# Optimization experiments

Measured on AMD Instinct MI355X. Metric: run time of the kernel, lower is better.

The kernel has to match this reference:

```python
import jax, jax.numpy as jnp
import numpy as np

IMAGE_SIZE = 256
DET = int(IMAGE_SIZE * 2 ** 0.5 + 0.5)  # 362 detector bins (diagonal coverage)
US = 4
N_ACQ = 45                     # acquired views: 0,4,...,176 degrees
N_FULL = (N_ACQ - 1) * US + 1  # 177 full (upsampled) views


def setup_inputs() -> dict:
    key = jax.random.key(0)
    k1, k2 = jax.random.split(key)
    x_source = jax.random.normal(k1, (2, 1, IMAGE_SIZE, IMAGE_SIZE), jnp.float32)
    s_target = jax.random.normal(k2, (2, 1, DET, N_ACQ), jnp.float32)
    theta_acq = np.arange(0, 180, 4, dtype=np.float64)  # 45 acquired angles
    segs = [np.linspace(theta_acq[i], theta_acq[i + 1], US + 1)[:-1] for i in range(N_ACQ - 1)]
    theta_full = np.concatenate(segs + [theta_acq[-1:]]).astype(np.float32)  # [177]
    acq_idx = (np.arange(N_ACQ) * US).astype(np.int32)  # positions of acquired angles in theta_full
    return {"x_source": x_source, "s_target": s_target,
            "thetas_deg": jnp.asarray(theta_full), "acq_idx": jnp.asarray(acq_idx)}


def bilinear_gather(img, xs, ys):
    # img: [B,C,H,W]; xs, ys: pixel coords [A,det,det]; zero outside the image.
    H, W = img.shape[-2], img.shape[-1]
    x0 = jnp.floor(xs); y0 = jnp.floor(ys)
    wx = xs - x0; wy = ys - y0
    x0i = x0.astype(jnp.int32); y0i = y0.astype(jnp.int32)

    def get(yi, xi):
        valid = (xi >= 0) & (xi < W) & (yi >= 0) & (yi < H)
        v = img[:, :, jnp.clip(yi, 0, H - 1), jnp.clip(xi, 0, W - 1)]  # [B,C,A,det,det]
        return jnp.where(valid, v, 0.0)

    return (get(y0i, x0i) * (1 - wy) * (1 - wx)
            + get(y0i, x0i + 1) * (1 - wy) * wx
            + get(y0i + 1, x0i) * wy * (1 - wx)
            + get(y0i + 1, x0i + 1) * wy * wx)


def radon(x, thetas_rad, det):
    # Ray-sum projection: sino[theta, t] = sum_s image(t*cos - s*sin, t*sin + s*cos)
    B, C, H, W = x.shape
    t = jnp.arange(det, dtype=x.dtype) - (det - 1) / 2.0  # centered detector/ray coord
    cos = jnp.cos(thetas_rad)[:, None, None]
    sin = jnp.sin(thetas_rad)[:, None, None]
    T = t[None, :, None]; S = t[None, None, :]
    xs = T * cos - S * sin + (W - 1) / 2.0  # [A,det,det]
    ys = T * sin + S * cos + (H - 1) / 2.0
    return bilinear_gather(x, xs, ys).sum(-1)  # [B,C,A,det]


def ramp_filter(size):
    # skimage/pytorch_radon style ramp built from its real-space kernel
    n = np.concatenate([np.arange(1, size // 2 + 1, 2), np.arange(size // 2 - 1, 0, -2)])
    f = np.zeros(size)
    f[0] = 0.25
    f[1::2] = -1.0 / (np.pi * n) ** 2
    return jnp.asarray(2 * np.real(np.fft.fft(f)), dtype=jnp.float32)


def fbp(sino, thetas_rad, image_size):
    # Filtered back-projection. sino: [B,C,det,A]
    B, C, det, A = sino.shape
    pad = max(64, int(2 ** np.ceil(np.log2(2 * det))))
    filt = ramp_filter(pad)  # [pad]
    sp = jnp.pad(sino, ((0, 0), (0, 0), (0, pad - det), (0, 0)))
    sf = jnp.fft.ifft(jnp.fft.fft(sp, axis=2) * filt[None, None, :, None], axis=2).real
    sf = jnp.transpose(sf[:, :, :det, :], (0, 1, 3, 2)).astype(sino.dtype)  # [B,C,A,det]
    g = jnp.arange(image_size, dtype=sino.dtype) - (image_size - 1) / 2.0
    cos = jnp.cos(thetas_rad); sin = jnp.sin(thetas_rad)
    # detector coordinate hit by each pixel, per angle: t = x*cos + y*sin
    t = (cos[:, None, None] * g[None, None, :]
         + sin[:, None, None] * g[None, :, None] + (det - 1) / 2.0)  # [A,H,W]
    t = t.reshape(A, -1)
    t0 = jnp.floor(t)
    w = t - t0
    t0i = t0.astype(jnp.int32)
    aidx = jnp.arange(A)[:, None]

    def samp(ti):
        valid = (ti >= 0) & (ti < det)
        return jnp.where(valid, sf[:, :, aidx, jnp.clip(ti, 0, det - 1)], 0.0)  # [B,C,A,HW]

    v = samp(t0i) * (1 - w) + samp(t0i + 1) * w
    reco = v.sum(2) * (jnp.pi / (2 * A))
    return reco.reshape(B, C, image_size, image_size)


def reference(x_source, s_target, thetas_deg, acq_idx):
    th = thetas_deg * (jnp.pi / 180.0)
    s = radon(x_source, th, DET)          # [B,C,A,det]
    s = jnp.transpose(s, (0, 1, 3, 2))    # [B,C,det,A] -- angle axis last, as in the module
    # masked data-consistency update: acquired columns become (target - predicted)
    s = s.at[..., acq_idx].set(s_target - s[..., acq_idx])
    return fbp(s, th, IMAGE_SIZE)
```

## Files before the change

### kernel.cpp

```cpp
#include <hip/hip_runtime.h>
#include <math.h>

#define IMG   256
#define NFULL 177
#define DETN  362
#define NACQ  45
#define PAD   1024

#define SINO_OFF 0
#define SF_OFF   131072

#define HALF_T 180.5f
#define SEGL   32
#define TILE_W 1664

__constant__ const int kStripOrd[46] =
    {22,23,21,24,20,25,19,26,18,27,17,28,16,29,15,30,14,31,13,32,
     12,33,11,34,10,35,9,36,8,37,7,38,6,39,5,40,4,41,3,42,2,43,1,44,0,45};

__device__ __forceinline__ void gload16(const float* g, float* l) {
    __builtin_amdgcn_global_load_lds(
        (const __attribute__((address_space(1))) void*)g,
        (__attribute__((address_space(3))) void*)l, 16, 0, 0);
}

template<int P>
__device__ __forceinline__ float2 radon_strip2(
    const float* __restrict__ img0,
    const float* __restrict__ img1,
    float* tb,
    const float c, const float s,
    const float xbase, const float ybase,
    const float xAB_mn, const float yAB_mn, const float yAB_mx,
    const int Slo, const int Shi, const int lane)
{
    constexpr int W4   = P / 4;
    constexpr int HMAX = TILE_W / P;
    const int ts = lane & 7;
    float val0 = 0.0f, val1 = 0.0f;

    for (int Sseg = Slo; Sseg < Shi; Sseg += SEGL) {
        const float sv0 = (float)Sseg - HALF_T;
        const float sv1 = sv0 + (float)(SEGL - 1);
        const float xmn = xAB_mn - sv1 * s;
        const float ya  = sv0 * c, yb = sv1 * c;
        const float ymn = yAB_mn + fminf(ya, yb);
        const float ymx = yAB_mx + fmaxf(ya, yb);
        const int ix0  = (int)floorf(xmn) - 1;
        const int iy0  = (int)floorf(ymn) - 1;
        const int ix0a = ix0 & ~3;
        const int h    = min((int)floorf(ymx) + 3 - iy0, HMAX);
        const int total4 = W4 * h;
        const int nfull  = total4 & ~63;
        const bool interior = (ix0a >= 0) & (iy0 >= 0) &
                              (ix0a + P <= IMG) & (iy0 + h <= IMG);

        asm volatile("s_waitcnt lgkmcnt(0)" ::: "memory");

        if (interior) {
            const int base0 = iy0 * IMG + ix0a;
            for (int f0 = 0; f0 < nfull; f0 += 64) {
                const int f  = f0 + lane;
                const int r  = f / W4;
                const int c4 = f - r * W4;
                const int go = base0 + r * IMG + (c4 << 2);
                gload16(img0 + go, tb + (f0 << 2));
                gload16(img1 + go, tb + TILE_W + (f0 << 2));
            }
            const int f = nfull + lane;
            if (f < total4) {
                const int r  = f / W4;
                const int c4 = f - r * W4;
                const int go = base0 + r * IMG + (c4 << 2);
                gload16(img0 + go, tb + (nfull << 2));
                gload16(img1 + go, tb + TILE_W + (nfull << 2));
            }
        } else {
            for (int f = lane; f < total4; f += 64) {
                const int r  = f / W4;
                const int c4 = f - r * W4;
                const int gy = iy0 + r;
                const int gx = ix0a + (c4 << 2);
                const bool ok = ((unsigned)gy < (unsigned)IMG) &
                                ((unsigned)gx <= (unsigned)(IMG - 4));
                float4 v0 = make_float4(0.f, 0.f, 0.f, 0.f);
                float4 v1 = v0;
                if (ok) {
                    const int go = gy * IMG + gx;
                    v0 = *(const float4*)(img0 + go);
                    v1 = *(const float4*)(img1 + go);
                }
                *(float4*)(tb + (f << 2)) = v0;
                *(float4*)(tb + TILE_W + (f << 2)) = v1;
            }
        }
        asm volatile("s_waitcnt vmcnt(0) lgkmcnt(0)" ::: "memory");
        __builtin_amdgcn_sched_barrier(0);

        const float xoff = xbase - (float)ix0a;
        const float yoff = ybase - (float)iy0;
        const int Send = min(Sseg + SEGL, Shi);

        auto samp = [&](float sval) {
            const float xs  = fmaf(-sval, s, xoff);
            const float ys  = fmaf(sval, c, yoff);
            const float x0f = floorf(xs);
            const float y0f = floorf(ys);
            const float wx  = xs - x0f;
            const float wy  = ys - y0f;
            const int base = (int)fmaf(y0f, (float)P, x0f);
            const float a00 = tb[base];
            const float a01 = tb[base + 1];
            const float a10 = tb[base + P];
            const float a11 = tb[base + P + 1];
            const float b00 = tb[TILE_W + base];
            const float b01 = tb[TILE_W + base + 1];
            const float b10 = tb[TILE_W + base + P];
            const float b11 = tb[TILE_W + base + P + 1];
            const float ah0 = fmaf(wx, a01 - a00, a00);
            const float ah1 = fmaf(wx, a11 - a10, a10);
            val0 += fmaf(wy, ah1 - ah0, ah0);
            const float bh0 = fmaf(wx, b01 - b00, b00);
            const float bh1 = fmaf(wx, b11 - b10, b10);
            val1 += fmaf(wy, bh1 - bh0, bh0);
        };

        if (Send - Sseg == SEGL) {
            const float s0 = (float)(Sseg + ts) - HALF_T;
            #pragma unroll
            for (int u = 0; u < SEGL / 8; ++u) samp(s0 + (float)(8 * u));
        } else {
            for (int S = Sseg + ts; S < Send; S += 8) samp((float)S - HALF_T);
        }
    }
    return make_float2(val0, val1);
}

__global__ __launch_bounds__(64, 4) void radon_kernel(
    const float* __restrict__ x,
    const float* __restrict__ thetas,
    float* __restrict__ sino)
{
    const int a = blockIdx.x;
    const int lane = threadIdx.x & 63;
    const int sp   = kStripOrd[blockIdx.y];
    const int T0   = sp << 3;
    const int tt   = lane >> 3;
    const int ts   = lane & 7;
    const int T    = T0 + tt;

    __shared__ __align__(16) float tile[2 * TILE_W];

    const float th = thetas[a] * (float)(M_PI / 180.0);
    const float c = cosf(th);
    const float s = sinf(th);
    const float cx = (IMG - 1) * 0.5f;
    const float cy = (IMG - 1) * 0.5f;
    const float Tc = (float)T - HALF_T;
    const float xbase = Tc * c + cx;
    const float ybase = Tc * s + cy;

    float lo = -1e30f, hi = 1e30f;
    bool empty = (T >= DETN);
    {   const float aa = -s;
        if (aa > 1e-5f)       { lo = fmaxf(lo, (-1.0f - xbase) / aa); hi = fminf(hi, (256.0f - xbase) / aa); }
        else if (aa < -1e-5f) { lo = fmaxf(lo, (256.0f - xbase) / aa); hi = fminf(hi, (-1.0f - xbase) / aa); }
        else if (xbase <= -1.0f || xbase >= 256.0f) empty = true;
    }
    {   const float aa = c;
        if (aa > 1e-5f)       { lo = fmaxf(lo, (-1.0f - ybase) / aa); hi = fminf(hi, (256.0f - ybase) / aa); }
        else if (aa < -1e-5f) { lo = fmaxf(lo, (256.0f - ybase) / aa); hi = fminf(hi, (-1.0f - ybase) / aa); }
        else if (ybase <= -1.0f || ybase >= 256.0f) empty = true;
    }
    lo = fmaxf(lo, -200.0f);
    hi = fminf(hi, 200.0f);
    int Slo = max(0, (int)floorf(lo + HALF_T) - 1);
    int Shi = min(DETN, (int)floorf(hi + HALF_T) + 2);
    if (empty || Shi < Slo) { Slo = 0; Shi = 0; }

    int wlo = (Shi > Slo) ? Slo : DETN;
    int whi = (Shi > Slo) ? Shi : 0;
    #pragma unroll
    for (int d = 1; d < 64; d <<= 1) {
        wlo = min(wlo, __shfl_xor(wlo, d, 64));
        whi = max(whi, __shfl_xor(whi, d, 64));
    }

    int best = 2;
    {
        const float ac = fabsf(c), as = fabsf(s);
        const float spanx = 7.f * ac + 31.f * as;
        const float spany = 7.f * as + 31.f * ac;
        const float Pc[6] = {36.f, 40.f, 44.f, 48.f, 52.f, 56.f};
        const int   Hm[6] = {46, 41, 37, 34, 32, 29};
        int bcost = 1 << 30;
        #pragma unroll
        for (int p = 0; p < 6; ++p) {
            const float Pf = Pc[p];
            const float dT = s * Pf + c;
            const float dS = c * Pf - s;
            const int bank = (int)floorf((float)tt * dT + (float)ts * dS + 0.5f) & 31;
            unsigned long long m = ~0ull;
            #pragma unroll
            for (int bit = 0; bit < 5; ++bit) {
                const unsigned long long bb = __ballot((bank >> bit) & 1);
                m &= ((bank >> bit) & 1) ? bb : ~bb;
            }
            int cnt = __popcll(m);
            #pragma unroll
            for (int d = 1; d < 64; d <<= 1) cnt = max(cnt, __shfl_xor(cnt, d, 64));
            const bool fit = (spanx <= Pf - 8.05f) && (spany <= (float)Hm[p] - 5.05f);
            if (fit && cnt < bcost) { bcost = cnt; best = p; }
        }
    }

    const float TcA = (float)T0 - HALF_T;
    const float TcB = (float)(T0 + 7) - HALF_T;
    const float xAB_mn = fminf(TcA * c + cx, TcB * c + cx);
    const float yAB_mn = fminf(TcA * s + cy, TcB * s + cy);
    const float yAB_mx = fmaxf(TcA * s + cy, TcB * s + cy);

    const float* __restrict__ img0 = x;
    const float* __restrict__ img1 = x + IMG * IMG;

    float2 val;
    switch (best) {
    case 0:  val = radon_strip2<36>(img0, img1, tile, c, s, xbase, ybase,
                                    xAB_mn, yAB_mn, yAB_mx, wlo, whi, lane); break;
    case 1:  val = radon_strip2<40>(img0, img1, tile, c, s, xbase, ybase,
                                    xAB_mn, yAB_mn, yAB_mx, wlo, whi, lane); break;
    case 2:  val = radon_strip2<44>(img0, img1, tile, c, s, xbase, ybase,
                                    xAB_mn, yAB_mn, yAB_mx, wlo, whi, lane); break;
    case 3:  val = radon_strip2<48>(img0, img1, tile, c, s, xbase, ybase,
                                    xAB_mn, yAB_mn, yAB_mx, wlo, whi, lane); break;
    case 4:  val = radon_strip2<52>(img0, img1, tile, c, s, xbase, ybase,
                                    xAB_mn, yAB_mn, yAB_mx, wlo, whi, lane); break;
    default: val = radon_strip2<56>(img0, img1, tile, c, s, xbase, ybase,
                                    xAB_mn, yAB_mn, yAB_mx, wlo, whi, lane); break;
    }

    val.x += __shfl_xor(val.x, 1, 8);
    val.x += __shfl_xor(val.x, 2, 8);
    val.x += __shfl_xor(val.x, 4, 8);
    val.y += __shfl_xor(val.y, 1, 8);
    val.y += __shfl_xor(val.y, 2, 8);
    val.y += __shfl_xor(val.y, 4, 8);
    if (ts == 0 && T < DETN) {
        sino[a * DETN + T] = val.x;
        sino[(NFULL + a) * DETN + T] = val.y;
    }
}

__global__ __launch_bounds__(192) void dc_filter_kernel(
    const float* __restrict__ sino,
    const float* __restrict__ st,
    const int*   __restrict__ acq,
    float* __restrict__ sf)
{
    const int blk = blockIdx.x;
    const int b = blk / NFULL;
    const int a = blk - b * NFULL;
    const int tid = threadIdx.x;

    __shared__ float col[DETN];
    __shared__ float gf[PAD];

    const float SC = (float)(M_PI / (2.0 * NFULL));
    const float c0 = 0.5f * SC;
    for (int n = tid; n < PAD; n += 192) {
        float v = 0.0f;
        if (n & 1) {
            const int d = (n < PAD - n) ? n : (PAD - n);
            const float pd = (float)M_PI * (float)d;
            v = -2.0f / (pd * pd) * SC;
        }
        gf[n] = v;
    }

    int inv = -1;
    for (int i = 0; i < NACQ; ++i) {
        if (acq[i] == a) inv = i;
    }

    for (int m = tid; m < DETN; m += 192) {
        float val = sino[(b * NFULL + a) * DETN + m];
        if (inv >= 0) {
            val = st[(b * DETN + m) * NACQ + inv] - val;
        }
        col[m] = val;
    }
    __syncthreads();

    const int T = blockIdx.y * 181 + tid;
    if (tid < 181) {
        const int m0 = (T + 1) & 1;
        float acc = c0 * col[T];
        #pragma unroll 4
        for (int k = 0; k < 181; ++k) {
            const int m = m0 + 2 * k;
            acc += col[m] * gf[(T - m) & (PAD - 1)];
        }
        sf[(b * NFULL + a) * DETN + T] = acc;
    }
}

__global__ __launch_bounds__(256) void backproject_kernel(
    const float* __restrict__ sf,
    const float* __restrict__ thetas,
    float* __restrict__ out)
{
    __shared__ float cb[2 * NFULL];
    __shared__ float red[256];
    const int tid = threadIdx.x;
    const int lane  = tid & 63;
    const int phase = tid >> 6;
    const int pix = blockIdx.x * 64 + lane;
    const int b = pix >> 16;
    const int y = (pix >> 8) & 255;
    const int xq = pix & 255;
    const float gx = (float)xq - (IMG - 1) * 0.5f;
    const float gy = (float)y  - (IMG - 1) * 0.5f;

    for (int a = tid; a < NFULL; a += 256) {
        float th = thetas[a] * (float)(M_PI / 180.0);
        cb[2 * a]     = cosf(th);
        cb[2 * a + 1] = fmaf(sinf(th), gy, HALF_T);
    }
    __syncthreads();

    const float* __restrict__ sfb = sf + b * NFULL * DETN;

    float acc = 0.0f;
    #pragma unroll 4
    for (int a = phase; a < NFULL; a += 4) {
        const float cs = cb[2 * a];
        const float bs = cb[2 * a + 1];
        const float t = fmaf(cs, gx, bs);
        const float t0f = floorf(t);
        const float w = t - t0f;
        const float* row = sfb + a * DETN + (int)t0f;
        const float v0 = row[0];
        const float v1 = row[1];
        acc += v0 + w * (v1 - v0);
    }
    red[tid] = acc;
    __syncthreads();
    if (tid < 64) {
        out[blockIdx.x * 64 + tid] =
            red[tid] + red[tid + 64] + red[tid + 128] + red[tid + 192];
    }
}

extern "C" void kernel_launch(void* const* d_in, const int* in_sizes, int n_in,
                              void* d_out, int out_size, void* d_ws, size_t ws_size,
                              hipStream_t stream) {
    const float* x      = (const float*)d_in[0];
    const float* st     = (const float*)d_in[1];
    const float* thetas = (const float*)d_in[2];
    const int*   acq    = (const int*)d_in[3];
    float* out  = (float*)d_out;
    float* wsf  = (float*)d_ws;
    float* sino = wsf + SINO_OFF;
    float* sf   = wsf + SF_OFF;

    dim3 gA(NFULL, 46);
    radon_kernel<<<gA, 64, 0, stream>>>(x, thetas, sino);
    dim3 gB(2 * NFULL, 2);
    dc_filter_kernel<<<gB, 192, 0, stream>>>(sino, st, acq, sf);
    backproject_kernel<<<(2 * IMG * IMG) / 64, 256, 0, stream>>>(sf, thetas, out);
}
```

Baseline: 123.5 us.

## Prefetch next radon tile segment into registers while sampling current one

Replaces the direct global-to-LDS tile loads with a software pipeline in the radon strip loop. The next segment's image window is loaded into per-lane float4 registers (clamped addresses) before the current segment is sampled, and committed to LDS with out-of-bounds zeroing at the start of the next iteration. The goal is to hide global-memory latency behind the bilinear sampling work of a single-wave block. In exchange it uses many more VGPRs for staging, so launch bounds drop from 4 to 3 waves per SIMD, and it loses the cheaper interior fast path.

```diff
diff --git a/kernel.cpp b/kernel.cpp
--- a/kernel.cpp
+++ b/kernel.cpp
@@ -17,12 +17,6 @@
 __constant__ const int kStripOrd[46] =
     {22,23,21,24,20,25,19,26,18,27,17,28,16,29,15,30,14,31,13,32,
      12,33,11,34,10,35,9,36,8,37,7,38,6,39,5,40,4,41,3,42,2,43,1,44,0,45};
-
-__device__ __forceinline__ void gload16(const float* g, float* l) {
-    __builtin_amdgcn_global_load_lds(
-        (const __attribute__((address_space(1))) void*)g,
-        (__attribute__((address_space(3))) void*)l, 16, 0, 0);
-}
 
 template<int P>
 __device__ __forceinline__ float2 radon_strip2(
@@ -34,12 +28,16 @@
     const float xAB_mn, const float yAB_mn, const float yAB_mx,
     const int Slo, const int Shi, const int lane)
 {
-    constexpr int W4   = P / 4;
-    constexpr int HMAX = TILE_W / P;
+    constexpr int W4    = P / 4;
+    constexpr int HMAX  = TILE_W / P;
+    constexpr int MAXCH = (TILE_W / 4 + 63) / 64;
     const int ts = lane & 7;
     float val0 = 0.0f, val1 = 0.0f;
-
-    for (int Sseg = Slo; Sseg < Shi; Sseg += SEGL) {
+    if (Slo >= Shi) return make_float2(0.0f, 0.0f);
+
+    float4 ra[MAXCH], rb[MAXCH];
+
+    auto window = [&](int Sseg) -> int4 {
         const float sv0 = (float)Sseg - HALF_T;
         const float sv1 = sv0 + (float)(SEGL - 1);
         const float xmn = xAB_mn - sv1 * s;
@@ -50,55 +48,66 @@
         const int iy0  = (int)floorf(ymn) - 1;
         const int ix0a = ix0 & ~3;
         const int h    = min((int)floorf(ymx) + 3 - iy0, HMAX);
-        const int total4 = W4 * h;
-        const int nfull  = total4 & ~63;
-        const bool interior = (ix0a >= 0) & (iy0 >= 0) &
-                              (ix0a + P <= IMG) & (iy0 + h <= IMG);
-
-        asm volatile("s_waitcnt lgkmcnt(0)" ::: "memory");
-
-        if (interior) {
-            const int base0 = iy0 * IMG + ix0a;
-            for (int f0 = 0; f0 < nfull; f0 += 64) {
-                const int f  = f0 + lane;
-                const int r  = f / W4;
-                const int c4 = f - r * W4;
-                const int go = base0 + r * IMG + (c4 << 2);
-                gload16(img0 + go, tb + (f0 << 2));
-                gload16(img1 + go, tb + TILE_W + (f0 << 2));
-            }
-            const int f = nfull + lane;
+        return make_int4(ix0a, iy0, h, W4 * h );
+    };
+
+    auto issue = [&](const int4 wp) {
+        const int total4 = wp.w;
+        #pragma unroll
+        for (int i = 0; i < MAXCH; ++i) {
+            const int f = i * 64 + lane;
             if (f < total4) {
                 const int r  = f / W4;
                 const int c4 = f - r * W4;
-                const int go = base0 + r * IMG + (c4 << 2);
-                gload16(img0 + go, tb + (nfull << 2));
-                gload16(img1 + go, tb + TILE_W + (nfull << 2));
+                const int py = min(max(wp.y + r, 0), IMG - 1);
+                const int px = min(max(wp.x + (c4 << 2), 0), IMG - 4);
+                const int go = py * IMG + px;
+                ra[i] = *(const float4*)(img0 + go);
+                rb[i] = *(const float4*)(img1 + go);
             }
-        } else {
-            for (int f = lane; f < total4; f += 64) {
+        }
+        __builtin_amdgcn_sched_barrier(0);
+    };
+
+    auto commit = [&](const int4 wp) {
+        const int total4 = wp.w;
+        #pragma unroll
+        for (int i = 0; i < MAXCH; ++i) {
+            const int f = i * 64 + lane;
+            if (f < total4) {
                 const int r  = f / W4;
                 const int c4 = f - r * W4;
-                const int gy = iy0 + r;
-                const int gx = ix0a + (c4 << 2);
+                const int gy = wp.y + r;
+                const int gx = wp.x + (c4 << 2);
                 const bool ok = ((unsigned)gy < (unsigned)IMG) &
                                 ((unsigned)gx <= (unsigned)(IMG - 4));
-                float4 v0 = make_float4(0.f, 0.f, 0.f, 0.f);
-                float4 v1 = v0;
-                if (ok) {
-                    const int go = gy * IMG + gx;
-                    v0 = *(const float4*)(img0 + go);
-                    v1 = *(const float4*)(img1 + go);
+                float4 v0 = ra[i], v1 = rb[i];
+                if (!ok) {
+                    v0 = make_float4(0.f, 0.f, 0.f, 0.f);
+                    v1 = make_float4(0.f, 0.f, 0.f, 0.f);
                 }
                 *(float4*)(tb + (f << 2)) = v0;
                 *(float4*)(tb + TILE_W + (f << 2)) = v1;
             }
         }
-        asm volatile("s_waitcnt vmcnt(0) lgkmcnt(0)" ::: "memory");
+    };
+
+    int4 wp = window(Slo);
+    issue(wp);
+
+    for (int Sseg = Slo; Sseg < Shi; Sseg += SEGL) {
+        asm volatile("s_waitcnt lgkmcnt(0)" ::: "memory");
+        commit(wp);
+        int4 wpn = wp;
+        if (Sseg + SEGL < Shi) {
+            wpn = window(Sseg + SEGL);
+            issue(wpn);
+        }
+        asm volatile("s_waitcnt lgkmcnt(0)" ::: "memory");
         __builtin_amdgcn_sched_barrier(0);
 
-        const float xoff = xbase - (float)ix0a;
-        const float yoff = ybase - (float)iy0;
+        const float xoff = xbase - (float)wp.x;
+        const float yoff = ybase - (float)wp.y;
         const int Send = min(Sseg + SEGL, Shi);
 
         auto samp = [&](float sval) {
@@ -132,11 +141,12 @@
         } else {
             for (int S = Sseg + ts; S < Send; S += 8) samp((float)S - HALF_T);
         }
+        wp = wpn;
     }
     return make_float2(val0, val1);
 }
 
-__global__ __launch_bounds__(64, 4) void radon_kernel(
+__global__ __launch_bounds__(64, 3) void radon_kernel(
     const float* __restrict__ x,
     const float* __restrict__ thetas,
     float* __restrict__ sino)
```

After: 127.8 us. +3.5%, slower.

## Pack four radon strip wavefronts per block and shrink per-segment LDS tiles

Applied to the files above, without the earlier changes.

The radon kernel now launches 256-thread blocks in which each of the four wavefronts handles its own detector strip, with a private LDS tile per wave. The segment length drops from 32 to 16 and the tile from 1664 to 640 floats, and the candidate tile pitches are cut down accordingly. The aim is more resident waves and fewer tiny blocks, which should hide gather latency better. The cost is more frequent tile reloads with smaller segments, plus padding entries that leave some waves idle.

```diff
diff --git a/kernel.cpp b/kernel.cpp
--- a/kernel.cpp
+++ b/kernel.cpp
@@ -11,12 +11,13 @@
 #define SF_OFF   131072
 
 #define HALF_T 180.5f
-#define SEGL   32
-#define TILE_W 1664
-
-__constant__ const int kStripOrd[46] =
-    {22,23,21,24,20,25,19,26,18,27,17,28,16,29,15,30,14,31,13,32,
-     12,33,11,34,10,35,9,36,8,37,7,38,6,39,5,40,4,41,3,42,2,43,1,44,0,45};
+#define SEGL   16
+#define TILE_W 640
+
+__constant__ const int kStripOrd4[48] =
+    {22,23,21,24, 20,25,19,26, 18,27,17,28, 16,29,15,30,
+     14,31,13,32, 12,33,11,34, 10,35, 9,36,  8,37, 7,38,
+      6,39, 5,40,  4,41, 3,42,  2,43, 1,44,  0,45,-1,-1};
 
 __device__ __forceinline__ void gload16(const float* g, float* l) {
     __builtin_amdgcn_global_load_lds(
@@ -136,20 +137,23 @@
     return make_float2(val0, val1);
 }
 
-__global__ __launch_bounds__(64, 4) void radon_kernel(
+__global__ __launch_bounds__(256, 8) void radon_kernel(
     const float* __restrict__ x,
     const float* __restrict__ thetas,
     float* __restrict__ sino)
 {
     const int a = blockIdx.x;
+    const int w    = threadIdx.x >> 6;
     const int lane = threadIdx.x & 63;
-    const int sp   = kStripOrd[blockIdx.y];
+    const int sp   = kStripOrd4[blockIdx.y * 4 + w];
+    if (sp < 0) return;
     const int T0   = sp << 3;
     const int tt   = lane >> 3;
     const int ts   = lane & 7;
     const int T    = T0 + tt;
 
-    __shared__ __align__(16) float tile[2 * TILE_W];
+    __shared__ __align__(16) float tile[4][2 * TILE_W];
+    float* tb = tile[w];
 
     const float th = thetas[a] * (float)(M_PI / 180.0);
     const float c = cosf(th);
@@ -189,13 +193,13 @@
     int best = 2;
     {
         const float ac = fabsf(c), as = fabsf(s);
-        const float spanx = 7.f * ac + 31.f * as;
-        const float spany = 7.f * as + 31.f * ac;
-        const float Pc[6] = {36.f, 40.f, 44.f, 48.f, 52.f, 56.f};
-        const int   Hm[6] = {46, 41, 37, 34, 32, 29};
+        const float spanx = 7.f * ac + 15.f * as;
+        const float spany = 7.f * as + 15.f * ac;
+        const float Pc[4] = {20.f, 24.f, 28.f, 32.f};
+        const int   Hm[4] = {32, 26, 22, 20};
         int bcost = 1 << 30;
         #pragma unroll
-        for (int p = 0; p < 6; ++p) {
+        for (int p = 0; p < 4; ++p) {
             const float Pf = Pc[p];
             const float dT = s * Pf + c;
             const float dS = c * Pf - s;
@@ -225,17 +229,13 @@
 
     float2 val;
     switch (best) {
-    case 0:  val = radon_strip2<36>(img0, img1, tile, c, s, xbase, ybase,
+    case 0:  val = radon_strip2<20>(img0, img1, tb, c, s, xbase, ybase,
                                     xAB_mn, yAB_mn, yAB_mx, wlo, whi, lane); break;
-    case 1:  val = radon_strip2<40>(img0, img1, tile, c, s, xbase, ybase,
+    case 1:  val = radon_strip2<24>(img0, img1, tb, c, s, xbase, ybase,
                                     xAB_mn, yAB_mn, yAB_mx, wlo, whi, lane); break;
-    case 2:  val = radon_strip2<44>(img0, img1, tile, c, s, xbase, ybase,
+    case 2:  val = radon_strip2<28>(img0, img1, tb, c, s, xbase, ybase,
                                     xAB_mn, yAB_mn, yAB_mx, wlo, whi, lane); break;
-    case 3:  val = radon_strip2<48>(img0, img1, tile, c, s, xbase, ybase,
-                                    xAB_mn, yAB_mn, yAB_mx, wlo, whi, lane); break;
-    case 4:  val = radon_strip2<52>(img0, img1, tile, c, s, xbase, ybase,
-                                    xAB_mn, yAB_mn, yAB_mx, wlo, whi, lane); break;
-    default: val = radon_strip2<56>(img0, img1, tile, c, s, xbase, ybase,
+    default: val = radon_strip2<32>(img0, img1, tb, c, s, xbase, ybase,
                                     xAB_mn, yAB_mn, yAB_mx, wlo, whi, lane); break;
     }
 
@@ -363,8 +363,8 @@
     float* sino = wsf + SINO_OFF;
     float* sf   = wsf + SF_OFF;
 
-    dim3 gA(NFULL, 46);
-    radon_kernel<<<gA, 64, 0, stream>>>(x, thetas, sino);
+    dim3 gA(NFULL, 12);
+    radon_kernel<<<gA, 256, 0, stream>>>(x, thetas, sino);
     dim3 gB(2 * NFULL, 2);
     dc_filter_kernel<<<gB, 192, 0, stream>>>(sino, st, acq, sf);
     backproject_kernel<<<(2 * IMG * IMG) / 64, 256, 0, stream>>>(sf, thetas, out);
```

After: 115.6 us. 1.07x faster.
